# Optimization experiments

Hardware: AMD Instinct MI355X
Metric: run time of the kernel (lower is better)

## Reference

```python
import jax, jax.numpy as jnp
import numpy as np

P = 512
H, W = 256, 256
TANFOVX = 0.5
TANFOVY = 0.5
NEAR = 0.2  # frustum near-plane cull as in 3DGS preprocess
COV_BLUR = 0.3  # low-pass filter added to 2D covariance diagonal (3DGS)
ALPHA_MIN = 1.0 / 255.0
ALPHA_MAX = 0.99


def quat_to_rotmat(q):
    # q: [P,4] normalized (r, x, y, z) -> [P,3,3]
    r, x, y, z = q[:, 0], q[:, 1], q[:, 2], q[:, 3]
    R = jnp.stack([
        1 - 2 * (y * y + z * z), 2 * (x * y - r * z), 2 * (x * z + r * y),
        2 * (x * y + r * z), 1 - 2 * (x * x + z * z), 2 * (y * z - r * x),
        2 * (x * z - r * y), 2 * (y * z + r * x), 1 - 2 * (x * x + y * y),
    ], axis=-1)
    return R.reshape(-1, 3, 3)


def setup_inputs() -> dict:
    key = jax.random.key(0)
    ks = jax.random.split(key, 6)
    # Gaussians in front of a camera at the origin looking down +z.
    xy = jax.random.uniform(ks[0], (P, 2), minval=-2.0, maxval=2.0)
    z = jax.random.uniform(ks[1], (P, 1), minval=2.0, maxval=6.0)
    means3D = jnp.concatenate([xy, z], axis=-1).astype(jnp.float32)
    opacities = jax.random.normal(ks[2], (P, 1), dtype=jnp.float32)  # logits
    scales = (jnp.log(0.05) + 0.3 * jax.random.normal(ks[3], (P, 3))).astype(jnp.float32)  # log-scales
    rotations = jax.random.normal(ks[4], (P, 4), dtype=jnp.float32)  # raw quats
    colors_precomp = jax.random.uniform(ks[5], (P, 3), dtype=jnp.float32)
    viewmatrix = jnp.eye(4, dtype=jnp.float32)
    n, f = NEAR, 100.0
    proj = np.zeros((4, 4), np.float32)
    proj[0, 0] = 1.0 / TANFOVX
    proj[1, 1] = 1.0 / TANFOVY
    proj[2, 2] = f / (f - n)
    proj[2, 3] = -f * n / (f - n)
    proj[3, 2] = 1.0
    projmatrix = jnp.asarray(proj)  # full (proj @ view) since view = I
    campos = jnp.zeros(3, jnp.float32)
    bg = jnp.zeros(3, jnp.float32)
    return dict(means3D=means3D, opacities=opacities, scales=scales,
                rotations=rotations, colors_precomp=colors_precomp,
                viewmatrix=viewmatrix, projmatrix=projmatrix, campos=campos, bg=bg)


def reference(means3D, opacities, scales, rotations, colors_precomp,
              viewmatrix, projmatrix, campos, bg):
    # --- activations applied by the autograd Function forward ---
    opa = jax.nn.sigmoid(opacities[:, 0])                      # [P]
    s = jnp.exp(scales)                                        # [P,3]
    q = rotations / jnp.clip(jnp.linalg.norm(rotations, axis=-1, keepdims=True), 1e-12)
    R = quat_to_rotmat(q)                                      # [P,3,3]
    # 3D covariance: cov = (R S)(R S)^T
    L = R * s[:, None, :]
    cov3D = jnp.einsum('pij,pkj->pik', L, L)                   # [P,3,3]
    # --- camera-space transform ---
    t = means3D @ viewmatrix[:3, :3].T + viewmatrix[:3, 3]     # [P,3]
    tx, ty, tz = t[:, 0], t[:, 1], t[:, 2]
    valid = tz > NEAR
    tzc = jnp.where(valid, tz, 1.0)
    limx, limy = 1.3 * TANFOVX, 1.3 * TANFOVY
    txz = jnp.clip(tx / tzc, -limx, limx) * tzc
    tyz = jnp.clip(ty / tzc, -limy, limy) * tzc
    fx = W / (2.0 * TANFOVX)
    fy = H / (2.0 * TANFOVY)
    # --- EWA splatting: 2D covariance = J W cov3D W^T J^T ---
    zeros = jnp.zeros_like(tzc)
    J = jnp.stack([
        jnp.stack([fx / tzc, zeros, -fx * txz / (tzc * tzc)], axis=-1),
        jnp.stack([zeros, fy / tzc, -fy * tyz / (tzc * tzc)], axis=-1),
    ], axis=-2)                                                # [P,2,3]
    T = jnp.einsum('pij,jk->pik', J, viewmatrix[:3, :3])       # [P,2,3]
    cov2D = jnp.einsum('pij,pjk,plk->pil', T, cov3D, T)        # [P,2,2]
    cov2D = cov2D + COV_BLUR * jnp.eye(2, dtype=cov2D.dtype)
    det = cov2D[:, 0, 0] * cov2D[:, 1, 1] - cov2D[:, 0, 1] ** 2
    det = jnp.where(det == 0.0, 1.0, det)
    conA = cov2D[:, 1, 1] / det
    conB = -cov2D[:, 0, 1] / det
    conC = cov2D[:, 0, 0] / det
    # --- projection to pixel coordinates ---
    ph = jnp.concatenate([means3D, jnp.ones((means3D.shape[0], 1), means3D.dtype)], -1) @ projmatrix.T
    pw = 1.0 / (ph[:, 3] + 1e-7)
    pix_x = ((ph[:, 0] * pw + 1.0) * W - 1.0) * 0.5            # [P]
    pix_y = ((ph[:, 1] * pw + 1.0) * H - 1.0) * 0.5
    # --- global front-to-back depth sort (stand-in for tile binning + per-tile sort) ---
    depth = jnp.where(valid, tz, jnp.inf)
    order = jnp.argsort(depth)
    opa_s = opa[order]
    conA_s, conB_s, conC_s = conA[order], conB[order], conC[order]
    px_s, py_s = pix_x[order], pix_y[order]
    valid_s = valid[order]
    col_s = colors_precomp[order]
    # --- dense alpha compositing over all pixels ---
    xg = jnp.arange(W, dtype=jnp.float32)
    yg = jnp.arange(H, dtype=jnp.float32)
    dx = px_s[:, None, None] - xg[None, None, :]               # [P,1,W]
    dy = py_s[:, None, None] - yg[None, :, None]               # [P,H,1]
    power = (-0.5 * (conA_s[:, None, None] * dx * dx + conC_s[:, None, None] * dy * dy)
             - conB_s[:, None, None] * dx * dy)                # [P,H,W]
    alpha = jnp.minimum(ALPHA_MAX, opa_s[:, None, None] * jnp.exp(power))
    alpha = jnp.where((power > 0.0) | (alpha < ALPHA_MIN) | (~valid_s[:, None, None]), 0.0, alpha)
    Tcum = jnp.cumprod(1.0 - alpha, axis=0)                    # [P,H,W]
    Tprev = jnp.concatenate([jnp.ones((1, H, W), alpha.dtype), Tcum[:-1]], axis=0)
    wgt = alpha * Tprev                                        # per-Gaussian compositing weight
    out_color = jnp.einsum('phw,pc->hwc', wgt, col_s) + Tcum[-1][..., None] * bg  # [H,W,3]
    return out_color
```

## Files before the change

kernel.cpp:

```cpp
#include <hip/hip_runtime.h>
#include <math.h>

#define PCOUNT 512
#define IMG_W 256
#define IMG_H 256
#define TANX 0.5f
#define TANY 0.5f
#define NEARP 0.2f
#define BLUR 0.3f
#define AMIN (1.0f/255.0f)
#define AMAX 0.99f

__global__ __launch_bounds__(1024) void fused_raster_kernel(
    const float* __restrict__ means, const float* __restrict__ opac,
    const float* __restrict__ scales, const float* __restrict__ rots,
    const float* __restrict__ cols, const float* __restrict__ vm,
    const float* __restrict__ pm, const float* __restrict__ bg,
    float* __restrict__ out)
{
    __shared__ float s_params[PCOUNT * 12];
    __shared__ float s_depth[PCOUNT];
    __shared__ unsigned short s_order[PCOUNT];
    __shared__ float4 s_part[4][256];
    __shared__ int s_wcnt[16];
    __shared__ int s_total;

    int t = threadIdx.x;
    int wave = t >> 6, lane = t & 63;
    int tileX = blockIdx.x & 15, tileY = blockIdx.x >> 4;
    float tx0 = (float)(tileX << 4), tx1 = tx0 + 15.0f;
    float ty0 = (float)(tileY << 4), ty1 = ty0 + 15.0f;

    bool hit = false;
    float conA = 0, conB = 0, conC = 0, px = 0, py = 0, opa_eff = 0, tz = 0;
    int g = t;
    if (t < PCOUNT) {
        float mx = means[3*g], my = means[3*g+1], mz = means[3*g+2];
        float o = 1.0f / (1.0f + __expf(-opac[g]));
        float sx = __expf(scales[3*g]), sy = __expf(scales[3*g+1]), sz = __expf(scales[3*g+2]);

        float qr = rots[4*g], qx = rots[4*g+1], qy = rots[4*g+2], qz = rots[4*g+3];
        float qn = fmaxf(sqrtf(qr*qr + qx*qx + qy*qy + qz*qz), 1e-12f);
        float qi = 1.0f/qn;
        qr *= qi; qx *= qi; qy *= qi; qz *= qi;

        float R00 = 1.0f-2.0f*(qy*qy+qz*qz), R01 = 2.0f*(qx*qy - qr*qz), R02 = 2.0f*(qx*qz + qr*qy);
        float R10 = 2.0f*(qx*qy + qr*qz), R11 = 1.0f-2.0f*(qx*qx+qz*qz), R12 = 2.0f*(qy*qz - qr*qx);
        float R20 = 2.0f*(qx*qz - qr*qy), R21 = 2.0f*(qy*qz + qr*qx), R22 = 1.0f-2.0f*(qx*qx+qy*qy);

        float s0 = sx*sx, s1 = sy*sy, s2 = sz*sz;
        float c00 = R00*R00*s0 + R01*R01*s1 + R02*R02*s2;
        float c01 = R00*R10*s0 + R01*R11*s1 + R02*R12*s2;
        float c02 = R00*R20*s0 + R01*R21*s1 + R02*R22*s2;
        float c11 = R10*R10*s0 + R11*R11*s1 + R12*R12*s2;
        float c12 = R10*R20*s0 + R11*R21*s1 + R12*R22*s2;
        float c22 = R20*R20*s0 + R21*R21*s1 + R22*R22*s2;

        float tvx = vm[0]*mx + vm[1]*my + vm[2]*mz + vm[3];
        float tvy = vm[4]*mx + vm[5]*my + vm[6]*mz + vm[7];
        tz = vm[8]*mx + vm[9]*my + vm[10]*mz + vm[11];
        bool valid = tz > NEARP;
        float tzc = valid ? tz : 1.0f;

        float limx = 1.3f*TANX, limy = 1.3f*TANY;
        float txz = fminf(fmaxf(tvx/tzc, -limx), limx)*tzc;
        float tyz = fminf(fmaxf(tvy/tzc, -limy), limy)*tzc;

        float fx = (float)IMG_W/(2.0f*TANX), fy = (float)IMG_H/(2.0f*TANY);
        float J00 = fx/tzc, J02 = -fx*txz/(tzc*tzc);
        float J11 = fy/tzc, J12 = -fy*tyz/(tzc*tzc);

        float T00 = J00*vm[0] + J02*vm[8];
        float T01 = J00*vm[1] + J02*vm[9];
        float T02 = J00*vm[2] + J02*vm[10];
        float T10 = J11*vm[4] + J12*vm[8];
        float T11 = J11*vm[5] + J12*vm[9];
        float T12 = J11*vm[6] + J12*vm[10];

        float M00 = T00*c00 + T01*c01 + T02*c02;
        float M01 = T00*c01 + T01*c11 + T02*c12;
        float M02 = T00*c02 + T01*c12 + T02*c22;
        float M10 = T10*c00 + T11*c01 + T12*c02;
        float M11 = T10*c01 + T11*c11 + T12*c12;
        float M12 = T10*c02 + T11*c12 + T12*c22;
        float v00 = M00*T00 + M01*T01 + M02*T02 + BLUR;
        float v01 = M00*T10 + M01*T11 + M02*T12;
        float v11 = M10*T10 + M11*T11 + M12*T12 + BLUR;

        float det = v00*v11 - v01*v01;
        det = (det == 0.0f) ? 1.0f : det;
        float idet = 1.0f/det;
        conA = v11*idet; conB = -v01*idet; conC = v00*idet;

        float ph0 = pm[0]*mx + pm[1]*my + pm[2]*mz + pm[3];
        float ph1 = pm[4]*mx + pm[5]*my + pm[6]*mz + pm[7];
        float ph3 = pm[12]*mx + pm[13]*my + pm[14]*mz + pm[15];
        float pw = 1.0f/(ph3 + 1e-7f);
        px = ((ph0*pw + 1.0f)*(float)IMG_W - 1.0f)*0.5f;
        py = ((ph1*pw + 1.0f)*(float)IMG_H - 1.0f)*0.5f;

        opa_eff = valid ? o : 0.0f;

        float oa = opa_eff * 255.0f;
        if (oa > 1.0f) {
            float r2 = 2.0f * __logf(oa);
            float dxm = sqrtf(r2 * v00) + 1.0f;
            float dym = sqrtf(r2 * v11) + 1.0f;
            hit = (px - dxm <= tx1) & (px + dxm >= tx0) &
                  (py - dym <= ty1) & (py + dym >= ty0);
        }
    }

    unsigned long long m = __ballot(hit);
    int rnk = __popcll(m & ((1ull << lane) - 1ull));
    if (lane == 0) s_wcnt[wave] = __popcll(m);
    __syncthreads();
    int off = 0;
    for (int w = 0; w < wave; ++w) off += s_wcnt[w];
    if (hit) {
        int slot = off + rnk;
        float* p = &s_params[slot * 12];
        p[0] = conA; p[1] = conB; p[2] = conC; p[3] = px;
        p[4] = py;   p[5] = opa_eff;
        p[6] = cols[3*g]; p[7] = cols[3*g+1]; p[8] = cols[3*g+2];
        s_depth[slot] = tz;
    }
    if (t == 0) {
        int s = 0;
        #pragma unroll
        for (int w = 0; w < 16; ++w) s += s_wcnt[w];
        s_total = s;
    }
    __syncthreads();
    int total = s_total;

    if (t < total) {
        float dk = s_depth[t];
        int rank = 0;
        for (int j = 0; j < total; ++j) {
            float dj = s_depth[j];
            rank += (int)((dj < dk) || (dj == dk && j < t));
        }
        s_order[rank] = (unsigned short)t;
    }
    __syncthreads();

    int p = t & 255, seg = t >> 8;
    int lx = p & 15, ly = p >> 4;
    float fxp = tx0 + (float)lx, fyp = ty0 + (float)ly;

    int seglen = (total + 3) >> 2;
    int i0 = seg * seglen;
    int i1 = min(i0 + seglen, total);

    float T = 1.0f, cr = 0.0f, cg = 0.0f, cb = 0.0f;
    for (int i = i0; i < i1; ++i) {
        int k = s_order[i];
        const float* pp = &s_params[k * 12];
        float4 p0 = *(const float4*)(pp);
        float4 p1 = *(const float4*)(pp + 4);
        float pb  = pp[8];
        float dx = p0.w - fxp;
        float dy = p1.x - fyp;
        float power = -0.5f*(p0.x*dx*dx + p0.z*dy*dy) - p0.y*dx*dy;
        if (power <= 0.0f) {
            float al = p1.y * __expf(power);
            if (al >= AMIN) {
                al = fminf(al, AMAX);
                float w = al * T;
                cr += w * p1.z;
                cg += w * p1.w;
                cb += w * pb;
                T *= (1.0f - al);
            }
        }
    }
    s_part[seg][p] = make_float4(cr, cg, cb, T);
    __syncthreads();

    if (t < 256) {
        float4 r0 = s_part[0][t], r1 = s_part[1][t], r2 = s_part[2][t], r3 = s_part[3][t];
        float Tt  = r0.w * r1.w * r2.w * r3.w;
        float ocr = r0.x + r0.w*(r1.x + r1.w*(r2.x + r2.w*r3.x));
        float ocg = r0.y + r0.w*(r1.y + r1.w*(r2.y + r2.w*r3.y));
        float ocb = r0.z + r0.w*(r1.z + r1.w*(r2.z + r2.w*r3.z));

        int x = (tileX << 4) + (t & 15), y = (tileY << 4) + (t >> 4);
        int o = (y*IMG_W + x)*3;
        out[o+0] = ocr + Tt*bg[0];
        out[o+1] = ocg + Tt*bg[1];
        out[o+2] = ocb + Tt*bg[2];
    }
}

extern "C" void kernel_launch(void* const* d_in, const int* in_sizes, int n_in,
                              void* d_out, int out_size, void* d_ws, size_t ws_size,
                              hipStream_t stream) {
    const float* means  = (const float*)d_in[0];
    const float* opac   = (const float*)d_in[1];
    const float* scales = (const float*)d_in[2];
    const float* rots   = (const float*)d_in[3];
    const float* cols   = (const float*)d_in[4];
    const float* vm     = (const float*)d_in[5];
    const float* pm     = (const float*)d_in[6];
    const float* bg     = (const float*)d_in[8];

    fused_raster_kernel<<<256, 1024, 0, stream>>>(
        means, opac, scales, rots, cols, vm, pm, bg, (float*)d_out);
}
```

Measured before the change: 10.63 us.

## Scatter params in depth order, split list into 8 segments, two pixels per thread

```diff
diff --git a/kernel.cpp b/kernel.cpp
--- a/kernel.cpp
+++ b/kernel.cpp
@@ -20,10 +20,8 @@
 {
     __shared__ float s_params[PCOUNT * 12];
     __shared__ float s_depth[PCOUNT];
-    __shared__ unsigned short s_order[PCOUNT];
-    __shared__ float4 s_part[4][256];
+    __shared__ float4 s_part[8][256];
     __shared__ int s_wcnt[16];
-    __shared__ int s_total;
 
     int t = threadIdx.x;
     int wave = t >> 6, lane = t & 63;
@@ -33,13 +31,19 @@
 
     bool hit = false;
     float conA = 0, conB = 0, conC = 0, px = 0, py = 0, opa_eff = 0, tz = 0;
+    float colr = 0, colg = 0, colb = 0;
     int g = t;
     if (t < PCOUNT) {
         float mx = means[3*g], my = means[3*g+1], mz = means[3*g+2];
-        float o = 1.0f / (1.0f + __expf(-opac[g]));
-        float sx = __expf(scales[3*g]), sy = __expf(scales[3*g+1]), sz = __expf(scales[3*g+2]);
-
-        float qr = rots[4*g], qx = rots[4*g+1], qy = rots[4*g+2], qz = rots[4*g+3];
+        float op = opac[g];
+        float sc0 = scales[3*g], sc1 = scales[3*g+1], sc2 = scales[3*g+2];
+        float4 q4 = *(const float4*)(rots + 4*g);
+        colr = cols[3*g]; colg = cols[3*g+1]; colb = cols[3*g+2];
+
+        float o = 1.0f / (1.0f + __expf(-op));
+        float sx = __expf(sc0), sy = __expf(sc1), sz = __expf(sc2);
+
+        float qr = q4.x, qx = q4.y, qy = q4.z, qz = q4.w;
         float qn = fmaxf(sqrtf(qr*qr + qx*qx + qy*qy + qz*qz), 1e-12f);
         float qi = 1.0f/qn;
         qr *= qi; qx *= qi; qy *= qi; qz *= qi;
@@ -115,81 +119,85 @@
     int rnk = __popcll(m & ((1ull << lane) - 1ull));
     if (lane == 0) s_wcnt[wave] = __popcll(m);
     __syncthreads();
-    int off = 0;
-    for (int w = 0; w < wave; ++w) off += s_wcnt[w];
+
+    int off = 0, total = 0;
+    #pragma unroll
+    for (int w = 0; w < 16; ++w) {
+        int c = s_wcnt[w];
+        off   += (w < wave) ? c : 0;
+        total += c;
+    }
+    int slot = off + rnk;
+    if (hit) s_depth[slot] = tz;
+    __syncthreads();
+
     if (hit) {
-        int slot = off + rnk;
-        float* p = &s_params[slot * 12];
-        p[0] = conA; p[1] = conB; p[2] = conC; p[3] = px;
-        p[4] = py;   p[5] = opa_eff;
-        p[6] = cols[3*g]; p[7] = cols[3*g+1]; p[8] = cols[3*g+2];
-        s_depth[slot] = tz;
-    }
-    if (t == 0) {
-        int s = 0;
-        #pragma unroll
-        for (int w = 0; w < 16; ++w) s += s_wcnt[w];
-        s_total = s;
-    }
-    __syncthreads();
-    int total = s_total;
-
-    if (t < total) {
-        float dk = s_depth[t];
         int rank = 0;
         for (int j = 0; j < total; ++j) {
             float dj = s_depth[j];
-            rank += (int)((dj < dk) || (dj == dk && j < t));
+            rank += (int)((dj < tz) || (dj == tz && j < slot));
         }
-        s_order[rank] = (unsigned short)t;
-    }
-    __syncthreads();
-
-    int p = t & 255, seg = t >> 8;
-    int lx = p & 15, ly = p >> 4;
-    float fxp = tx0 + (float)lx, fyp = ty0 + (float)ly;
-
-    int seglen = (total + 3) >> 2;
+        float* p = &s_params[rank * 12];
+        p[0] = conA; p[1] = conB; p[2] = conC; p[3] = px;
+        p[4] = py;   p[5] = opa_eff;
+        p[6] = colr; p[7] = colg; p[8] = colb;
+    }
+    __syncthreads();
+
+    int p0i = t & 127, seg = t >> 7;
+    int lx0 = p0i & 15, ly0 = p0i >> 4;
+    int ly1 = (p0i + 128) >> 4;
+    float fx0 = tx0 + (float)lx0;
+    float fy0 = ty0 + (float)ly0, fy1 = ty0 + (float)ly1;
+
+    int seglen = (total + 7) >> 3;
     int i0 = seg * seglen;
     int i1 = min(i0 + seglen, total);
 
-    float T = 1.0f, cr = 0.0f, cg = 0.0f, cb = 0.0f;
+    float Ta = 1.0f, ar = 0.0f, ag = 0.0f, ab = 0.0f;
+    float Tb = 1.0f, br = 0.0f, bgn = 0.0f, bb = 0.0f;
     for (int i = i0; i < i1; ++i) {
-        int k = s_order[i];
-        const float* pp = &s_params[k * 12];
-        float4 p0 = *(const float4*)(pp);
-        float4 p1 = *(const float4*)(pp + 4);
-        float pb  = pp[8];
-        float dx = p0.w - fxp;
-        float dy = p1.x - fyp;
-        float power = -0.5f*(p0.x*dx*dx + p0.z*dy*dy) - p0.y*dx*dy;
-        if (power <= 0.0f) {
-            float al = p1.y * __expf(power);
-            if (al >= AMIN) {
-                al = fminf(al, AMAX);
-                float w = al * T;
-                cr += w * p1.z;
-                cg += w * p1.w;
-                cb += w * pb;
-                T *= (1.0f - al);
-            }
+        const float* pp = &s_params[i * 12];
+        float4 q0 = *(const float4*)(pp);
+        float4 q1 = *(const float4*)(pp + 4);
+        float qb  = pp[8];
+
+        float dx = q0.w - fx0;
+        float dya = q1.x - fy0, dyb = q1.x - fy1;
+
+        float pwa = -0.5f*(q0.x*dx*dx + q0.z*dya*dya) - q0.y*dx*dya;
+        float pwb = -0.5f*(q0.x*dx*dx + q0.z*dyb*dyb) - q0.y*dx*dyb;
+
+        float ala = q1.y * __expf(pwa);
+        float alb = q1.y * __expf(pwb);
+        ala = ((pwa <= 0.0f) & (ala >= AMIN)) ? fminf(ala, AMAX) : 0.0f;
+        alb = ((pwb <= 0.0f) & (alb >= AMIN)) ? fminf(alb, AMAX) : 0.0f;
+
+        float wa = ala * Ta, wb = alb * Tb;
+        ar += wa * q1.z;  ag += wa * q1.w;  ab += wa * qb;
+        br += wb * q1.z;  bgn += wb * q1.w; bb += wb * qb;
+        Ta *= (1.0f - ala);
+        Tb *= (1.0f - alb);
+    }
+    s_part[seg][p0i]       = make_float4(ar, ag, ab, Ta);
+    s_part[seg][p0i + 128] = make_float4(br, bgn, bb, Tb);
+    __syncthreads();
+
+    if (t < 256) {
+        float4 acc = s_part[7][t];
+        #pragma unroll
+        for (int s = 6; s >= 0; --s) {
+            float4 r = s_part[s][t];
+            acc.x = r.x + r.w * acc.x;
+            acc.y = r.y + r.w * acc.y;
+            acc.z = r.z + r.w * acc.z;
+            acc.w = r.w * acc.w;
         }
-    }
-    s_part[seg][p] = make_float4(cr, cg, cb, T);
-    __syncthreads();
-
-    if (t < 256) {
-        float4 r0 = s_part[0][t], r1 = s_part[1][t], r2 = s_part[2][t], r3 = s_part[3][t];
-        float Tt  = r0.w * r1.w * r2.w * r3.w;
-        float ocr = r0.x + r0.w*(r1.x + r1.w*(r2.x + r2.w*r3.x));
-        float ocg = r0.y + r0.w*(r1.y + r1.w*(r2.y + r2.w*r3.y));
-        float ocb = r0.z + r0.w*(r1.z + r1.w*(r2.z + r2.w*r3.z));
-
         int x = (tileX << 4) + (t & 15), y = (tileY << 4) + (t >> 4);
         int o = (y*IMG_W + x)*3;
-        out[o+0] = ocr + Tt*bg[0];
-        out[o+1] = ocg + Tt*bg[1];
-        out[o+2] = ocb + Tt*bg[2];
+        out[o+0] = acc.x + acc.w*bg[0];
+        out[o+1] = acc.y + acc.w*bg[1];
+        out[o+2] = acc.z + acc.w*bg[2];
     }
 }
 
```

Measured after the change: 10.86 us. 2.2% more time.
